# Kernel optimization log

Hardware: AMD Instinct MI355X
Metric: run time of the kernel (lower is better)

Reference implementation:

```python
import jax, jax.numpy as jnp
import numpy as np

N, M, C, L, T = 1024, 64, 512, 64, 8192
EPS = 1e-16


def setup_inputs() -> dict:
    key = jax.random.key(0)
    ks = jax.random.split(key, 9)
    sc = 0.05
    return {
        "sequence": jax.random.uniform(ks[0], (T, L), dtype=jnp.float32),
        "Wc": jax.random.normal(ks[1], (L + M, C), jnp.float32) * sc,
        "bc": jnp.zeros((C,), jnp.float32),
        "Wr": jax.random.normal(ks[2], (C, M + 6), jnp.float32) * sc,
        "br": jnp.zeros((M + 6,), jnp.float32),
        "Ww": jax.random.normal(ks[3], (C, 3 * M + 6), jnp.float32) * sc,
        "bw": jnp.zeros((3 * M + 6,), jnp.float32),
        "Wo": jax.random.normal(ks[4], (M, L), jnp.float32) * sc,
        "bo": jnp.zeros((L,), jnp.float32),
    }


def _address(Mt, k, beta, g, sh, gamma, w_prev):
    # content addressing: cosine similarity of key against each memory row
    sim = (Mt @ k) / (jnp.linalg.norm(Mt, axis=1) * jnp.linalg.norm(k) + EPS)
    wc = jax.nn.softmax(beta * sim)                      # [N]
    wg = g * wc + (1.0 - g) * w_prev                     # interpolation
    # circular convolution with 3-tap shift kernel (-1, 0, +1)
    ws = sh[0] * jnp.roll(wg, 1) + sh[1] * wg + sh[2] * jnp.roll(wg, -1)
    wsh = ws ** gamma                                    # sharpening
    return wsh / (jnp.sum(wsh) + EPS)


def _head_params(o):
    k = jnp.tanh(o[:M])
    beta = jax.nn.softplus(o[M])
    g = jax.nn.sigmoid(o[M + 1])
    sh = jax.nn.softmax(o[M + 2:M + 5])
    gamma = 1.0 + jax.nn.softplus(o[M + 5])
    return k, beta, g, sh, gamma


def reference(sequence, Wc, bc, Wr, br, Ww, bw, Wo, bo):
    M0 = jnp.full((N, M), 1e-06, jnp.float32)            # memory_bias
    w0 = jnp.zeros((N,), jnp.float32).at[N // 2].set(1.0)  # weight_bias
    r0 = jnp.full((M,), 1e-06, jnp.float32)              # read_bias

    def step(carry, s):
        Mt, ww, rw, r = carry
        h = jnp.tanh(jnp.concatenate([s, r]) @ Wc + bc)  # controller
        # write head: k, beta, g, shift, gamma, erase, add
        ow = h @ Ww + bw
        k, beta, g, sh, gamma = _head_params(ow)
        e = jax.nn.sigmoid(ow[M + 6:2 * M + 6])
        a = jnp.tanh(ow[2 * M + 6:])
        ww_n = _address(Mt, k, beta, g, sh, gamma, ww)
        Mt = Mt * (1.0 - ww_n[:, None] * e[None, :]) + ww_n[:, None] * a[None, :]
        # read head
        orr = h @ Wr + br
        k, beta, g, sh, gamma = _head_params(orr)
        rw_n = _address(Mt, k, beta, g, sh, gamma, rw)
        r_n = rw_n @ Mt                                  # [M]
        s_out = jnp.clip(r_n @ Wo + bo, 0.0, 1.0)
        return (Mt, ww_n, rw_n, r_n), (s_out, ww_n, rw_n, a, r_n)

    _, (seq_out, ww_h, rw_h, a_h, r_h) = jax.lax.scan(step, (M0, w0, w0, r0), sequence)
    return seq_out, ww_h, rw_h, a_h, r_h
```

## Files before the change

kernel.cpp:

```cpp
#include <hip/hip_runtime.h>
#include <math.h>

#define NN 1024
#define MM 64
#define CC 512
#define LL 64
#define TT 8192
#define EPSF 1e-16f

#define OFF_SEQ 0
#define OFF_WW  (TT*LL)
#define OFF_RW  (OFF_WW + TT*NN)
#define OFF_A   (OFF_RW + TT*NN)
#define OFF_R   (OFF_A + TT*MM)

#define WSF_PRE   0
#define WSF_M     (TT*CC)
#define WSF_WCAT  (WSF_M + 32768)

#define BAR() asm volatile("s_waitcnt lgkmcnt(0)\n\ts_barrier" ::: "memory")

__device__ __forceinline__ float sigmoid_f(float x) { return 1.0f / (1.0f + __expf(-x)); }
__device__ __forceinline__ float softplus_f(float x) { return (x > 15.0f) ? x : __logf(1.0f + __expf(x)); }
__device__ __forceinline__ float tanh_f(float x) { float e = __expf(2.0f * x); return 1.0f - 2.0f / (e + 1.0f); }
__device__ __forceinline__ float pow_f(float b, float g) { return __expf(g * __logf(b)); }
__device__ __forceinline__ int bitrev4(int l) {
    return ((l & 1) << 3) | ((l & 2) << 1) | ((l & 4) >> 1) | ((l & 8) >> 3);
}

__device__ __forceinline__ float xor_any(float v, const int m, const int lane) {
    if (m == 1)
        return __int_as_float(__builtin_amdgcn_mov_dpp(__float_as_int(v), 0xB1, 0xF, 0xF, true));
    if (m == 2)
        return __int_as_float(__builtin_amdgcn_mov_dpp(__float_as_int(v), 0x4E, 0xF, 0xF, true));
    return __shfl_xor(v, m, 64);
}

template<int CTRL>
__device__ __forceinline__ float dpp_add(float s) {
    int sh = __builtin_amdgcn_update_dpp(0, __float_as_int(s), CTRL, 0xF, 0xF, false);
    return s + __int_as_float(sh);
}
__device__ __forceinline__ float rowsum64(float s) {
    s = dpp_add<0x111>(s);
    s = dpp_add<0x112>(s);
    s = dpp_add<0x114>(s);
    s = dpp_add<0x118>(s);
    s = dpp_add<0x142>(s);
    s = dpp_add<0x143>(s);
    return s;
}

__global__ void pre_kernel(const float* __restrict__ seq, const float* __restrict__ Wc,
                           const float* __restrict__ bc, float* __restrict__ pre) {
    int gid = blockIdx.x * blockDim.x + threadIdx.x;
    int t = gid >> 9;
    int j = gid & 511;
    if (t >= TT) return;
    const float* s = seq + t * LL;
    float acc = bc[j];
    #pragma unroll 8
    for (int i = 0; i < LL; ++i) acc += s[i] * Wc[i * CC + j];
    pre[gid] = acc;
}

__global__ void pack_kernel(const float* __restrict__ Ww, const float* __restrict__ Wr,
                            float* __restrict__ Wcat) {
    int gid = blockIdx.x * 256 + threadIdx.x;
    if (gid >= 512 * 272) return;
    int r = gid / 272, c = gid - r * 272;
    float v = 0.0f;
    if (c < 198) v = Ww[r * 198 + c];
    else if (c < 268) v = Wr[r * 70 + (c - 198)];
    Wcat[gid] = v;
}

#define WOT_S 68
__global__ __launch_bounds__(1024)
void ntm_kernel(
    const float* __restrict__ pre,
    const float* __restrict__ Wc,
    const float* __restrict__ Wcat,
    const float* __restrict__ br,
    const float* __restrict__ bw,
    const float* __restrict__ Wo,
    const float* __restrict__ bo,
    float* __restrict__ out)
{
    __shared__ __align__(16) float sh_part[4096];
    __shared__ __align__(16) float sh_h[CC];
    __shared__ __align__(16) float sh_kw[MM];
    __shared__ __align__(16) float sh_kr[MM];
    __shared__ __align__(16) float sh_e[MM];
    __shared__ __align__(16) float sh_a[MM];
    __shared__ __align__(16) float sh_scal[16];
    __shared__ __align__(16) float2 sh_evwp[NN];
    __shared__ __align__(16) float red[4][16];
    __shared__ __align__(16) float wmat[16][MM];
    __shared__ __align__(16) float sh_r[MM];
    __shared__ __align__(16) float sh_WoT[LL * WOT_S];
    __shared__ __align__(16) float sh_bo[LL];
    __shared__ __align__(16) float sh_bw[200];
    __shared__ __align__(16) float sh_br[72];
    __shared__ __align__(16) float sh_pren[CC];

    const int tid  = threadIdx.x;
    const int lane = tid & 63;
    const int wv   = tid >> 6;

    for (int idx = tid; idx < MM * LL; idx += NN) {
        int i = idx >> 6, o = idx & 63;
        sh_WoT[o * WOT_S + i] = Wo[i * LL + o];
    }
    if (tid < LL)  sh_bo[tid] = bo[tid];
    if (tid < 198) sh_bw[tid] = bw[tid];
    if (tid < 70)  sh_br[tid] = br[tid];
    if (tid < MM)  sh_r[tid] = 1e-6f;
    if (tid < CC)  sh_pren[tid] = pre[tid];

    float Mlo[32];
    #pragma unroll
    for (int j = 0; j < 32; ++j) Mlo[j] = 1e-6f;
    float4 mh[8];
    #pragma unroll
    for (int k = 0; k < 8; ++k) mh[k] = make_float4(1e-6f, 1e-6f, 1e-6f, 1e-6f);
    float rown = sqrtf(64.0f * 1e-12f);
    float wwprev = (tid == NN / 2) ? 1.0f : 0.0f;
    float rwprev = wwprev;
    __syncthreads();

    for (int t = 0; t < TT; ++t) {
        {
            int g = tid & 127, q = tid >> 7;
            const float4* wbase = (const float4*)(Wc + (64 + q * 8) * CC) + g;
            float4 ra = *(const float4*)(sh_r + q * 8);
            float4 rb = *(const float4*)(sh_r + q * 8 + 4);
            float rv[8] = {ra.x, ra.y, ra.z, ra.w, rb.x, rb.y, rb.z, rb.w};
            float4 acc = make_float4(0.0f, 0.0f, 0.0f, 0.0f);
            #pragma unroll
            for (int i = 0; i < 8; ++i) {
                float4 w = wbase[i * 128];
                acc.x += rv[i] * w.x; acc.y += rv[i] * w.y;
                acc.z += rv[i] * w.z; acc.w += rv[i] * w.w;
            }
            ((float4*)sh_part)[q * 128 + g] = acc;
        }
        BAR();
        if (tid < CC) {
            float p0 = sh_part[tid]          + sh_part[512 + tid];
            float p1 = sh_part[1024 + tid]   + sh_part[1536 + tid];
            float p2 = sh_part[2048 + tid]   + sh_part[2560 + tid];
            float p3 = sh_part[3072 + tid]   + sh_part[3584 + tid];
            float v = sh_pren[tid] + ((p0 + p1) + (p2 + p3));
            sh_h[tid] = tanh_f(v);
        }
        BAR();
        if (tid < 544) {
            int g = tid % 68, q = tid / 68;
            const float4* wbase = (const float4*)(Wcat + (q * 64) * 272) + g;
            const float4* h4p = (const float4*)(sh_h + q * 64);
            float4 acc = make_float4(0.0f, 0.0f, 0.0f, 0.0f);
            #pragma unroll 2
            for (int i4 = 0; i4 < 16; ++i4) {
                float4 h4 = h4p[i4];
                const float4* wr = wbase + (i4 * 4) * 68;
                float4 w0 = wr[0];
                float4 w1 = wr[68];
                float4 w2 = wr[136];
                float4 w3 = wr[204];
                acc.x += h4.x * w0.x; acc.y += h4.x * w0.y; acc.z += h4.x * w0.z; acc.w += h4.x * w0.w;
                acc.x += h4.y * w1.x; acc.y += h4.y * w1.y; acc.z += h4.y * w1.z; acc.w += h4.y * w1.w;
                acc.x += h4.z * w2.x; acc.y += h4.z * w2.y; acc.z += h4.z * w2.z; acc.w += h4.z * w2.w;
                acc.x += h4.w * w3.x; acc.y += h4.w * w3.y; acc.z += h4.w * w3.z; acc.w += h4.w * w3.w;
            }
            ((float4*)sh_part)[q * 68 + g] = acc;
        } else if (wv == 15) {
            if (t > 0) {
                const float4* r4p = (const float4*)sh_r;
                const float4* wop = (const float4*)(sh_WoT + lane * WOT_S);
                float a0 = 0.0f, a1 = 0.0f;
                #pragma unroll
                for (int i4 = 0; i4 < 16; ++i4) {
                    float4 r = r4p[i4];
                    float4 w = wop[i4];
                    a0 += r.x * w.x + r.y * w.y;
                    a1 += r.z * w.z + r.w * w.w;
                }
                float acc = sh_bo[lane] + a0 + a1;
                out[OFF_SEQ + (t - 1) * LL + lane] = fminf(fmaxf(acc, 0.0f), 1.0f);
            }
        }
        BAR();
        float pren_v = 0.0f;
        #define OWV(c) ( (((sh_part[(c)] + sh_part[272 + (c)]) + (sh_part[544 + (c)] + sh_part[816 + (c)])) \
                        + ((sh_part[1088 + (c)] + sh_part[1360 + (c)]) + (sh_part[1632 + (c)] + sh_part[1904 + (c)]))) \
                        + ((c) < 198 ? sh_bw[(c)] : sh_br[(c) - 198]) )
        if (wv == 0) {
            float v = tanh_f(OWV(lane));
            sh_kw[lane] = v;
            float s2 = rowsum64(v * v);
            if (lane == 63) sh_scal[6] = sqrtf(s2);
        } else if (wv == 1) {
            float v = tanh_f(OWV(198 + lane));
            sh_kr[lane] = v;
            float s2 = rowsum64(v * v);
            if (lane == 63) sh_scal[14] = sqrtf(s2);
        } else if (wv == 2) {
            sh_e[lane] = sigmoid_f(OWV(70 + lane));
        } else if (wv == 3) {
            float v = tanh_f(OWV(134 + lane));
            sh_a[lane] = v;
            out[OFF_A + t * MM + lane] = v;
        } else if (wv == 4) {
            if (lane == 0) {
                sh_scal[0] = softplus_f(OWV(64));
                sh_scal[1] = sigmoid_f(OWV(65));
                float x0 = OWV(66), x1 = OWV(67), x2 = OWV(68);
                float mx = fmaxf(x0, fmaxf(x1, x2));
                float e0 = __expf(x0 - mx), e1 = __expf(x1 - mx), e2 = __expf(x2 - mx);
                float ss = e0 + e1 + e2;
                sh_scal[2] = e0 / ss; sh_scal[3] = e1 / ss; sh_scal[4] = e2 / ss;
                sh_scal[5] = 1.0f + softplus_f(OWV(69));
            }
        } else if (wv == 5) {
            if (lane == 0) {
                sh_scal[8] = softplus_f(OWV(198 + 64));
                sh_scal[9] = sigmoid_f(OWV(198 + 65));
                float x0 = OWV(198 + 66), x1 = OWV(198 + 67), x2 = OWV(198 + 68);
                float mx = fmaxf(x0, fmaxf(x1, x2));
                float e0 = __expf(x0 - mx), e1 = __expf(x1 - mx), e2 = __expf(x2 - mx);
                float ss = e0 + e1 + e2;
                sh_scal[10] = e0 / ss; sh_scal[11] = e1 / ss; sh_scal[12] = e2 / ss;
                sh_scal[13] = 1.0f + softplus_f(OWV(198 + 69));
            }
        } else if (wv >= 6 && wv < 14) {
            if (t + 1 < TT) pren_v = pre[(t + 1) * CC + (tid - 384)];
        }
        #undef OWV
        BAR();

        float betaW = sh_scal[0], gW = sh_scal[1];
        float s0W = sh_scal[2], s1W = sh_scal[3], s2W = sh_scal[4];
        float gamW = sh_scal[5], knW = sh_scal[6];
        {
            const float4* k4 = (const float4*)sh_kw;
            float d0 = 0.0f, d1 = 0.0f, d2 = 0.0f, d3 = 0.0f;
            #pragma unroll
            for (int j4 = 0; j4 < 8; ++j4) {
                float4 k = k4[j4];
                d0 += Mlo[4*j4]   * k.x;
                d1 += Mlo[4*j4+1] * k.y;
                d2 += Mlo[4*j4+2] * k.z;
                d3 += Mlo[4*j4+3] * k.w;
            }
            #pragma unroll
            for (int k8 = 0; k8 < 8; ++k8) {
                float4 k = k4[8 + k8];
                d0 += mh[k8].x * k.x;
                d1 += mh[k8].y * k.y;
                d2 += mh[k8].z * k.z;
                d3 += mh[k8].w * k.w;
            }
            float dot = (d0 + d1) + (d2 + d3);
            float sim = dot / (rown * knW + EPSF);
            float ev = __expf(betaW * sim);
            sh_evwp[tid] = make_float2(ev, wwprev);
            float s = rowsum64(ev);
            if (lane == 63) red[0][wv] = s;
        }
        BAR();
        float wshW;
        {
            const float4* rp = (const float4*)red[0];
            float Sev = 0.0f;
            #pragma unroll
            for (int w4 = 0; w4 < 4; ++w4) { float4 p = rp[w4]; Sev += p.x + p.y + p.z + p.w; }
            int tm1 = (tid + NN - 1) & (NN - 1), tp1 = (tid + 1) & (NN - 1);
            float2 em1 = sh_evwp[tm1], ec = sh_evwp[tid], ep1 = sh_evwp[tp1];
            float cEV = s0W * em1.x + s1W * ec.x + s2W * ep1.x;
            float cWP = s0W * em1.y + s1W * ec.y + s2W * ep1.y;
            float ws = (gW / Sev) * cEV + (1.0f - gW) * cWP;
            wshW = pow_f(ws, gamW);
            float s = rowsum64(wshW);
            if (lane == 63) red[1][wv] = s;
        }
        BAR();
        {
            const float4* rp = (const float4*)red[1];
            float Swsh = 0.0f;
            #pragma unroll
            for (int w4 = 0; w4 < 4; ++w4) { float4 p = rp[w4]; Swsh += p.x + p.y + p.z + p.w; }
            float wwn = wshW / (Swsh + EPSF);
            out[OFF_WW + t * NN + tid] = wwn;
            wwprev = wwn;
            const float4* e4p = (const float4*)sh_e;
            const float4* a4p = (const float4*)sh_a;
            float n0 = 0.0f, n1 = 0.0f, n2 = 0.0f, n3 = 0.0f;
            #pragma unroll
            for (int j4 = 0; j4 < 8; ++j4) {
                float4 e = e4p[j4], a = a4p[j4];
                float m0 = Mlo[4*j4]   * (1.0f - wwn * e.x) + wwn * a.x;
                float m1 = Mlo[4*j4+1] * (1.0f - wwn * e.y) + wwn * a.y;
                float m2 = Mlo[4*j4+2] * (1.0f - wwn * e.z) + wwn * a.z;
                float m3 = Mlo[4*j4+3] * (1.0f - wwn * e.w) + wwn * a.w;
                Mlo[4*j4] = m0; Mlo[4*j4+1] = m1; Mlo[4*j4+2] = m2; Mlo[4*j4+3] = m3;
                n0 += m0 * m0; n1 += m1 * m1; n2 += m2 * m2; n3 += m3 * m3;
            }
            #pragma unroll
            for (int k = 0; k < 8; ++k) {
                float4 e = e4p[8 + k], a = a4p[8 + k];
                float4 m = mh[k];
                m.x = m.x * (1.0f - wwn * e.x) + wwn * a.x;
                m.y = m.y * (1.0f - wwn * e.y) + wwn * a.y;
                m.z = m.z * (1.0f - wwn * e.z) + wwn * a.z;
                m.w = m.w * (1.0f - wwn * e.w) + wwn * a.w;
                mh[k] = m;
                n0 += m.x * m.x; n1 += m.y * m.y; n2 += m.z * m.z; n3 += m.w * m.w;
            }
            rown = sqrtf((n0 + n1) + (n2 + n3));
        }

        float betaR = sh_scal[8], gR = sh_scal[9];
        float s0R = sh_scal[10], s1R = sh_scal[11], s2R = sh_scal[12];
        float gamR = sh_scal[13], knR = sh_scal[14];
        {
            const float4* k4 = (const float4*)sh_kr;
            float d0 = 0.0f, d1 = 0.0f, d2 = 0.0f, d3 = 0.0f;
            #pragma unroll
            for (int j4 = 0; j4 < 8; ++j4) {
                float4 k = k4[j4];
                d0 += Mlo[4*j4]   * k.x;
                d1 += Mlo[4*j4+1] * k.y;
                d2 += Mlo[4*j4+2] * k.z;
                d3 += Mlo[4*j4+3] * k.w;
            }
            #pragma unroll
            for (int k8 = 0; k8 < 8; ++k8) {
                float4 k = k4[8 + k8];
                d0 += mh[k8].x * k.x;
                d1 += mh[k8].y * k.y;
                d2 += mh[k8].z * k.z;
                d3 += mh[k8].w * k.w;
            }
            float dot = (d0 + d1) + (d2 + d3);
            float sim = dot / (rown * knR + EPSF);
            float ev = __expf(betaR * sim);
            sh_evwp[tid] = make_float2(ev, rwprev);
            float s = rowsum64(ev);
            if (lane == 63) red[2][wv] = s;
        }
        BAR();
        float wshR;
        {
            const float4* rp = (const float4*)red[2];
            float Sev = 0.0f;
            #pragma unroll
            for (int w4 = 0; w4 < 4; ++w4) { float4 p = rp[w4]; Sev += p.x + p.y + p.z + p.w; }
            int tm1 = (tid + NN - 1) & (NN - 1), tp1 = (tid + 1) & (NN - 1);
            float2 em1 = sh_evwp[tm1], ec = sh_evwp[tid], ep1 = sh_evwp[tp1];
            float cEV = s0R * em1.x + s1R * ec.x + s2R * ep1.x;
            float cWP = s0R * em1.y + s1R * ec.y + s2R * ep1.y;
            float ws = (gR / Sev) * cEV + (1.0f - gR) * cWP;
            wshR = pow_f(ws, gamR);
            float s = rowsum64(wshR);
            if (lane == 63) red[3][wv] = s;
            #pragma unroll
            for (int chunk = 0; chunk < 4; ++chunk) {
                const int cb = chunk * 16;
                float v[16];
                if (chunk < 2) {
                    #pragma unroll
                    for (int i = 0; i < 16; ++i) v[i] = wshR * Mlo[chunk * 16 + i];
                } else {
                    #pragma unroll
                    for (int k = 0; k < 4; ++k) {
                        float4 m = mh[(chunk - 2) * 4 + k];
                        v[4*k]   = wshR * m.x;
                        v[4*k+1] = wshR * m.y;
                        v[4*k+2] = wshR * m.z;
                        v[4*k+3] = wshR * m.w;
                    }
                }
                #pragma unroll
                for (int st = 0; st < 4; ++st) {
                    const int m = 1 << st;
                    const int hs = 8 >> st;
                    bool hi = (lane & m) != 0;
                    #pragma unroll
                    for (int i = 0; i < 8; ++i) {
                        if (i < hs) {
                            float send = hi ? v[i] : v[i + hs];
                            float recv = xor_any(send, m, lane);
                            float keep = hi ? v[i + hs] : v[i];
                            v[i] = keep + recv;
                        }
                    }
                }
                float v0 = v[0];
                v0 += xor_any(v0, 16, lane);
                v0 += xor_any(v0, 32, lane);
                if (lane < 16) wmat[wv][cb + bitrev4(lane)] = v0;
            }
        }
        BAR();
        {
            if (wv >= 6 && wv < 14 && t + 1 < TT) sh_pren[tid - 384] = pren_v;
            const float4* rp = (const float4*)red[3];
            float Swsh = 0.0f;
            #pragma unroll
            for (int w4 = 0; w4 < 4; ++w4) { float4 p = rp[w4]; Swsh += p.x + p.y + p.z + p.w; }
            float inv = 1.0f / (Swsh + EPSF);
            float rwn = wshR * inv;
            out[OFF_RW + t * NN + tid] = rwn;
            rwprev = rwn;
            if (tid < MM) {
                float rv = 0.0f;
                #pragma unroll
                for (int w = 0; w < 16; ++w) rv += wmat[w][tid];
                rv *= inv;
                sh_r[tid] = rv;
                out[OFF_R + t * MM + tid] = rv;
            }
        }
        BAR();
    }

    if (tid < LL) {
        const float4* r4p = (const float4*)sh_r;
        const float4* wop = (const float4*)(sh_WoT + tid * WOT_S);
        float a0 = 0.0f, a1 = 0.0f;
        #pragma unroll
        for (int i4 = 0; i4 < 16; ++i4) {
            float4 r = r4p[i4];
            float4 w = wop[i4];
            a0 += r.x * w.x + r.y * w.y;
            a1 += r.z * w.z + r.w * w.w;
        }
        float acc = sh_bo[tid] + a0 + a1;
        out[OFF_SEQ + (TT - 1) * LL + tid] = fminf(fmaxf(acc, 0.0f), 1.0f);
    }
}

extern "C" void kernel_launch(void* const* d_in, const int* in_sizes, int n_in,
                              void* d_out, int out_size, void* d_ws, size_t ws_size,
                              hipStream_t stream) {
    const float* seq = (const float*)d_in[0];
    const float* Wc  = (const float*)d_in[1];
    const float* bc  = (const float*)d_in[2];
    const float* Wr  = (const float*)d_in[3];
    const float* br  = (const float*)d_in[4];
    const float* Ww  = (const float*)d_in[5];
    const float* bw  = (const float*)d_in[6];
    const float* Wo  = (const float*)d_in[7];
    const float* bo  = (const float*)d_in[8];
    float* out = (float*)d_out;

    float* wsf  = (float*)d_ws;
    float* pre  = wsf + WSF_PRE;
    float* Wcat = wsf + WSF_WCAT;

    pre_kernel<<<(TT * CC) / 256, 256, 0, stream>>>(seq, Wc, bc, pre);
    pack_kernel<<<(512 * 272 + 255) / 256, 256, 0, stream>>>(Ww, Wr, Wcat);
    ntm_kernel<<<1, 1024, 0, stream>>>(pre, Wc, Wcat, br, bw, Wo, bo, out);
}
```

Before: 129.4 ms.

## Spread head-projection GEMV across all 16 waves and move output projection later

The h·[Ww|Wr] projection used to run on 544 threads, each summing over 64 rows. It now runs on all 16 waves, each covering 32 rows: a lane computes one float4 column group, and the 4 leftover column groups are handled by a 16-lane shuffle reduction. This halves the serial inner loop per thread, which sits on the sequential critical path of every timestep. The cost is doubling the partial sums combined in OWV to 16 and enlarging sh_part. The Wo output projection moves to wave 15 in the following phase, where that wave is idle.

```diff
diff --git a/kernel.cpp b/kernel.cpp
--- a/kernel.cpp
+++ b/kernel.cpp
@@ -87,7 +87,7 @@
     const float* __restrict__ bo,
     float* __restrict__ out)
 {
-    __shared__ __align__(16) float sh_part[4096];
+    __shared__ __align__(16) float sh_part[4352];
     __shared__ __align__(16) float sh_h[CC];
     __shared__ __align__(16) float sh_kw[MM];
     __shared__ __align__(16) float sh_kr[MM];
@@ -155,45 +155,56 @@
             sh_h[tid] = tanh_f(v);
         }
         BAR();
-        if (tid < 544) {
-            int g = tid % 68, q = tid / 68;
-            const float4* wbase = (const float4*)(Wcat + (q * 64) * 272) + g;
-            const float4* h4p = (const float4*)(sh_h + q * 64);
-            float4 acc = make_float4(0.0f, 0.0f, 0.0f, 0.0f);
-            #pragma unroll 2
-            for (int i4 = 0; i4 < 16; ++i4) {
-                float4 h4 = h4p[i4];
-                const float4* wr = wbase + (i4 * 4) * 68;
-                float4 w0 = wr[0];
-                float4 w1 = wr[68];
-                float4 w2 = wr[136];
-                float4 w3 = wr[204];
-                acc.x += h4.x * w0.x; acc.y += h4.x * w0.y; acc.z += h4.x * w0.z; acc.w += h4.x * w0.w;
-                acc.x += h4.y * w1.x; acc.y += h4.y * w1.y; acc.z += h4.y * w1.z; acc.w += h4.y * w1.w;
-                acc.x += h4.z * w2.x; acc.y += h4.z * w2.y; acc.z += h4.z * w2.z; acc.w += h4.z * w2.w;
-                acc.x += h4.w * w3.x; acc.y += h4.w * w3.y; acc.z += h4.w * w3.z; acc.w += h4.w * w3.w;
-            }
-            ((float4*)sh_part)[q * 68 + g] = acc;
-        } else if (wv == 15) {
-            if (t > 0) {
-                const float4* r4p = (const float4*)sh_r;
-                const float4* wop = (const float4*)(sh_WoT + lane * WOT_S);
-                float a0 = 0.0f, a1 = 0.0f;
+        {
+            const int q = wv >> 1, half = wv & 1;
+            const int rowbase = q * 64 + half * 32;
+            {
+                const float4* wbase = (const float4*)(Wcat + rowbase * 272) + lane;
+                const float4* h4p = (const float4*)(sh_h + rowbase);
+                float4 acc = make_float4(0.0f, 0.0f, 0.0f, 0.0f);
+                #pragma unroll 4
+                for (int i4 = 0; i4 < 8; ++i4) {
+                    float4 h4 = h4p[i4];
+                    const float4* wr = wbase + (i4 * 4) * 68;
+                    float4 w0 = wr[0];
+                    float4 w1 = wr[68];
+                    float4 w2 = wr[136];
+                    float4 w3 = wr[204];
+                    acc.x += h4.x * w0.x; acc.y += h4.x * w0.y; acc.z += h4.x * w0.z; acc.w += h4.x * w0.w;
+                    acc.x += h4.y * w1.x; acc.y += h4.y * w1.y; acc.z += h4.y * w1.z; acc.w += h4.y * w1.w;
+                    acc.x += h4.z * w2.x; acc.y += h4.z * w2.y; acc.z += h4.z * w2.z; acc.w += h4.z * w2.w;
+                    acc.x += h4.w * w3.x; acc.y += h4.w * w3.y; acc.z += h4.w * w3.z; acc.w += h4.w * w3.w;
+                }
+                ((float4*)sh_part)[wv * 68 + lane] = acc;
+            }
+            {
+                const int g2 = 64 + (lane >> 4);
+                const int r0 = rowbase + (lane & 15) * 2;
+                const float4* wp = (const float4*)(Wcat + r0 * 272) + g2;
+                float4 wA = wp[0];
+                float4 wB = wp[68];
+                float hA = sh_h[r0], hB = sh_h[r0 + 1];
+                float4 p;
+                p.x = hA * wA.x + hB * wB.x;
+                p.y = hA * wA.y + hB * wB.y;
+                p.z = hA * wA.z + hB * wB.z;
+                p.w = hA * wA.w + hB * wB.w;
                 #pragma unroll
-                for (int i4 = 0; i4 < 16; ++i4) {
-                    float4 r = r4p[i4];
-                    float4 w = wop[i4];
-                    a0 += r.x * w.x + r.y * w.y;
-                    a1 += r.z * w.z + r.w * w.w;
+                for (int m = 1; m <= 8; m <<= 1) {
+                    p.x += xor_any(p.x, m, lane);
+                    p.y += xor_any(p.y, m, lane);
+                    p.z += xor_any(p.z, m, lane);
+                    p.w += xor_any(p.w, m, lane);
                 }
-                float acc = sh_bo[lane] + a0 + a1;
-                out[OFF_SEQ + (t - 1) * LL + lane] = fminf(fmaxf(acc, 0.0f), 1.0f);
+                if ((lane & 15) == 0) ((float4*)sh_part)[wv * 68 + g2] = p;
             }
         }
         BAR();
         float pren_v = 0.0f;
-        #define OWV(c) ( (((sh_part[(c)] + sh_part[272 + (c)]) + (sh_part[544 + (c)] + sh_part[816 + (c)])) \
-                        + ((sh_part[1088 + (c)] + sh_part[1360 + (c)]) + (sh_part[1632 + (c)] + sh_part[1904 + (c)]))) \
+        #define OWV(c) ( ( (((sh_part[(c)] + sh_part[272 + (c)]) + (sh_part[544 + (c)] + sh_part[816 + (c)])) \
+                          + ((sh_part[1088 + (c)] + sh_part[1360 + (c)]) + (sh_part[1632 + (c)] + sh_part[1904 + (c)]))) \
+                          + (((sh_part[2176 + (c)] + sh_part[2448 + (c)]) + (sh_part[2720 + (c)] + sh_part[2992 + (c)])) \
+                          + ((sh_part[3264 + (c)] + sh_part[3536 + (c)]) + (sh_part[3808 + (c)] + sh_part[4080 + (c)]))) ) \
                         + ((c) < 198 ? sh_bw[(c)] : sh_br[(c) - 198]) )
         if (wv == 0) {
             float v = tanh_f(OWV(lane));
@@ -235,6 +246,21 @@
             }
         } else if (wv >= 6 && wv < 14) {
             if (t + 1 < TT) pren_v = pre[(t + 1) * CC + (tid - 384)];
+        } else if (wv == 15) {
+            if (t > 0) {
+                const float4* r4p = (const float4*)sh_r;
+                const float4* wop = (const float4*)(sh_WoT + lane * WOT_S);
+                float a0 = 0.0f, a1 = 0.0f;
+                #pragma unroll
+                for (int i4 = 0; i4 < 16; ++i4) {
+                    float4 r = r4p[i4];
+                    float4 w = wop[i4];
+                    a0 += r.x * w.x + r.y * w.y;
+                    a1 += r.z * w.z + r.w * w.w;
+                }
+                float acc = sh_bo[lane] + a0 + a1;
+                out[OFF_SEQ + (t - 1) * LL + lane] = fminf(fmaxf(acc, 0.0f), 1.0f);
+            }
         }
         #undef OWV
         BAR();
```

Result: slower. 181.5 ms (+40.2%).
